# Performance work log

Measured on AMD Instinct MI355X. Metric: run time of the kernel, lower is better.

## Reference

```python
import jax, jax.numpy as jnp
import numpy as np

OUT_STEPS = 32
UNITS = 512
FEATURES = 64


def setup_inputs() -> dict:
    key = jax.random.key(0)
    ks = jax.random.split(key, 4)
    B, T, F, U = 2048, 128, FEATURES, UNITS
    scale = 0.05
    return {
        "inputs": jax.random.normal(ks[0], (B, T, F), dtype=jnp.float32),
        "W_x": jax.random.normal(ks[1], (F, 4 * U), dtype=jnp.float32) * scale,
        "W_h": jax.random.normal(ks[2], (U, 4 * U), dtype=jnp.float32) * scale,
        "b": jnp.zeros((4 * U,), dtype=jnp.float32),
        "dense_W": jax.random.normal(ks[3], (U, F), dtype=jnp.float32) * scale,
        "dense_b": jnp.zeros((F,), dtype=jnp.float32),
    }


def reference(inputs, W_x, W_h, b, dense_W, dense_b):
    U = W_h.shape[0]
    B = inputs.shape[0]

    def cell(h, c, x):
        # Keras LSTMCell: gates in i, f, g(c), o order
        z = x @ W_x + h @ W_h + b  # [B, 4U]
        i, f, g, o = jnp.split(z, 4, axis=-1)
        i = jax.nn.sigmoid(i)
        f = jax.nn.sigmoid(f)
        g = jnp.tanh(g)
        o = jax.nn.sigmoid(o)
        c2 = f * c + i * g
        h2 = o * jnp.tanh(c2)
        return h2, c2

    h0 = jnp.zeros((B, U), inputs.dtype)
    c0 = jnp.zeros((B, U), inputs.dtype)

    def warm_step(carry, x_t):
        h, c = carry
        h, c = cell(h, c, x_t)
        return (h, c), None

    (h, c), _ = jax.lax.scan(warm_step, (h0, c0), jnp.swapaxes(inputs, 0, 1))
    pred = h @ dense_W + dense_b  # [B, F]

    def dec_step(carry, _):
        p, hh, cc = carry
        hh, cc = cell(hh, cc, p)
        p2 = hh @ dense_W + dense_b
        return (p2, hh, cc), p2

    _, rest = jax.lax.scan(dec_step, (pred, h, c), None, length=OUT_STEPS - 1)
    preds = jnp.concatenate([pred[None], rest], axis=0)  # [out_steps, B, F]
    return jnp.swapaxes(preds, 0, 1)  # [B, out_steps, F]
```

## Files before the change

kernel.cpp:

```cpp
#include <hip/hip_runtime.h>
#include <hip/hip_bf16.h>

#define B_ 2048
#define T_ 128
#define F_ 64
#define U_ 512
#define FOURU 2048
#define OUTS 32
#define ROWS 128
#define COLSB 128
#define KTOT 576
#define LDSTR 584

typedef __attribute__((ext_vector_type(8))) short bf16x8;
typedef __attribute__((ext_vector_type(4))) float f32x4;

#define OFF_CNT   0
#define OFF_HBUF  20480
#define OFF_WT    (OFF_HBUF + 2*B_*U_*2)
#define OFF_WDEC  (OFF_WT + FOURU*KTOT*2)
#define OFF_DWT   (OFF_WDEC + FOURU*U_*2)
#define OFF_BDEC  (OFF_DWT + F_*U_*2)
#define OFF_XBF   (OFF_BDEC + FOURU*4)
#define WS_TOTAL  (OFF_XBF + (size_t)T_*B_*F_*2)

__device__ __forceinline__ short f2bf(float f) {
  union { float f; unsigned u; } a; a.f = f;
  unsigned u = a.u;
  unsigned r = u + 0x7FFFu + ((u >> 16) & 1u);
  return (short)(r >> 16);
}
__device__ __forceinline__ float sigm(float x){ return 1.0f/(1.0f+__expf(-x)); }
__device__ __forceinline__ float tanh_(float x){ return 1.0f - 2.0f/(1.0f+__expf(2.0f*x)); }

__global__ void prep_wt(const float* __restrict__ Wx, const float* __restrict__ Wh,
                        short* __restrict__ Wt) {
  int idx = blockIdx.x*256 + threadIdx.x;
  if (idx >= FOURU*KTOT) return;
  int c = idx / KTOT, k = idx % KTOT;
  float v = (k < F_) ? Wx[(size_t)k*FOURU + c] : Wh[(size_t)(k-F_)*FOURU + c];
  Wt[idx] = f2bf(v);
}
__global__ void prep_wdec(const float* __restrict__ Wh, const float* __restrict__ Wx,
                          const float* __restrict__ Dw, short* __restrict__ Wdec) {
  int idx = blockIdx.x*256 + threadIdx.x;
  if (idx >= FOURU*U_) return;
  int c = idx / U_, u = idx % U_;
  float a = Wh[(size_t)u*FOURU + c];
  for (int f=0; f<F_; ++f) a += Dw[u*F_ + f] * Wx[(size_t)f*FOURU + c];
  Wdec[idx] = f2bf(a);
}
__global__ void prep_bdec(const float* __restrict__ bv, const float* __restrict__ db,
                          const float* __restrict__ Wx, float* __restrict__ bdec) {
  int c = blockIdx.x*256 + threadIdx.x;
  if (c >= FOURU) return;
  float a = bv[c];
  for (int f=0; f<F_; ++f) a += db[f]*Wx[(size_t)f*FOURU + c];
  bdec[c] = a;
}
__global__ void prep_dwt(const float* __restrict__ Dw, short* __restrict__ Dwt) {
  int idx = blockIdx.x*256 + threadIdx.x;
  if (idx >= F_*U_) return;
  int f = idx / U_, u = idx % U_;
  Dwt[idx] = f2bf(Dw[u*F_ + f]);
}
__global__ void prep_x(const float* __restrict__ in, short* __restrict__ xbf) {
  int idx = blockIdx.x*256 + threadIdx.x;
  if (idx >= T_*B_*F_) return;
  int f = idx % F_, b = (idx / F_) % B_, t = idx / (F_*B_);
  xbf[idx] = f2bf(in[((size_t)b*T_ + t)*F_ + f]);
}

__global__ __launch_bounds__(1024, 4) void lstm_main(
    const short* __restrict__ xbf, const short* __restrict__ Wt,
    const short* __restrict__ Wdec, const short* __restrict__ Dwt,
    const float* __restrict__ bvec, const float* __restrict__ bdec,
    const float* __restrict__ dbv, short* hbuf, unsigned* cnt,
    float* __restrict__ out)
{
  __shared__ short wlds[COLSB*LDSTR];
  __shared__ int sSame;
  const int tid = threadIdx.x;
  const int bidx = blockIdx.x;
  const int gb = (bidx & 7)*2 + (bidx >> 7);
  const int gu = (bidx >> 3) & 15;

  unsigned* flags   = cnt + gb*256;
  unsigned* myFlag  = flags + gu*16;
  unsigned* regCnt  = cnt + 4096 + gb*16;
  unsigned* xcdTab  = cnt + 4352 + gb*16;
  unsigned* stepCnt = cnt + 4608 + gb*16;

  {
    unsigned xcc;
    asm volatile("s_getreg_b32 %0, hwreg(HW_REG_XCC_ID)" : "=s"(xcc));
    if (tid == 0) {
      __hip_atomic_store(&xcdTab[gu], xcc + 1u, __ATOMIC_RELAXED, __HIP_MEMORY_SCOPE_AGENT);
      __hip_atomic_fetch_add(regCnt, 1u, __ATOMIC_RELEASE, __HIP_MEMORY_SCOPE_AGENT);
      while (__hip_atomic_fetch_add(regCnt, 0u, __ATOMIC_RELAXED, __HIP_MEMORY_SCOPE_AGENT) < 16u)
        __builtin_amdgcn_s_sleep(1);
      __builtin_amdgcn_fence(__ATOMIC_ACQUIRE, "agent");
      unsigned x0 = __hip_atomic_load(&xcdTab[0], __ATOMIC_RELAXED, __HIP_MEMORY_SCOPE_AGENT);
      int same = 1;
      for (int i = 1; i < 16; ++i)
        same &= (__hip_atomic_load(&xcdTab[i], __ATOMIC_RELAXED, __HIP_MEMORY_SCOPE_AGENT) == x0);
      sSame = same;
    }
  }

  {
    const int c = tid >> 3, q = tid & 7;
    const int gate = (c >> 4) & 3;
    const int u = gu*32 + ((c >> 6) << 4) + (c & 15);
    const int gcol = gate*512 + u;
    const short* src = Wt + (size_t)gcol*KTOT + q*72;
    short* dst = wlds + c*LDSTR + q*72;
    #pragma unroll
    for (int j=0;j<9;j++)
      *(bf16x8*)(dst + j*8) = *(const bf16x8*)(src + j*8);
  }
  __syncthreads();
  const bool fastSync = (sSame != 0);

  const int w = tid >> 6, lane = tid & 63;
  const int wm = w >> 1, wn = w & 1;
  const int l15 = lane & 15, kh = lane >> 4;

  const int ucol = gu*32 + wn*16 + l15;
  float bia[4], biaD[4];
  #pragma unroll
  for (int g=0; g<4; ++g){ bia[g] = bvec[g*512 + ucol]; biaD[g] = bdec[g*512 + ucol]; }

  float cst[4] = {};
  const int rowA = gb*ROWS + wm*16 + l15;

  f32x4 acc[4];
  {
    const short* xp = xbf + ((size_t)0*B_ + rowA)*F_ + kh*8;
    bf16x8 a0 = *(const bf16x8*)(xp);
    bf16x8 a1 = *(const bf16x8*)(xp + 32);
    #pragma unroll
    for (int g=0; g<4; ++g) {
      bf16x8 b0 = *(const bf16x8*)(wlds + (size_t)(wn*64 + 16*g + l15)*LDSTR + kh*8);
      bf16x8 b1 = *(const bf16x8*)(wlds + (size_t)(wn*64 + 16*g + l15)*LDSTR + 32 + kh*8);
      f32x4 z = {0.f,0.f,0.f,0.f};
      z = __builtin_amdgcn_mfma_f32_16x16x32_bf16(a0, b0, z, 0,0,0);
      acc[g] = __builtin_amdgcn_mfma_f32_16x16x32_bf16(a1, b1, z, 0,0,0);
    }
  }

  for (int t = 0; t < 160; ++t) {
    if (t > 0) {
      if (fastSync) {
        if (tid < 64) {
          unsigned* fl = flags + (tid & 15)*16;
          for (;;) {
            unsigned v = __hip_atomic_load(fl, __ATOMIC_RELAXED, __HIP_MEMORY_SCOPE_AGENT);
            if (__ballot(v >= (unsigned)t) == ~0ull) break;
            __builtin_amdgcn_s_sleep(1);
          }
          asm volatile("buffer_inv sc0" ::: "memory");
          asm volatile("s_waitcnt vmcnt(0)" ::: "memory");
        }
      } else {
        if (tid == 0) {
          const unsigned target = 16u*(unsigned)t;
          while (__hip_atomic_fetch_add(stepCnt, 0u, __ATOMIC_RELAXED, __HIP_MEMORY_SCOPE_AGENT) < target)
            __builtin_amdgcn_s_sleep(1);
          __builtin_amdgcn_fence(__ATOMIC_ACQUIRE, "agent");
        }
      }
      __syncthreads();
    }

    if (t >= 128) {
      const int s = t - 128;
      if (gu < 8 && w < 4) {
        const short* hb = hbuf + (size_t)(t & 1)*B_*U_;
        const int pr0 = gb*ROWS + gu*16 + l15;
        f32x4 pa = {0.f,0.f,0.f,0.f};
        #pragma unroll
        for (int ks=0; ks<16; ++ks) {
          bf16x8 a = *(const bf16x8*)(hb + (size_t)pr0*U_ + ks*32 + kh*8);
          bf16x8 b = *(const bf16x8*)(Dwt + (size_t)(w*16 + l15)*U_ + ks*32 + kh*8);
          pa = __builtin_amdgcn_mfma_f32_16x16x32_bf16(a, b, pa, 0,0,0);
        }
        const int col = w*16 + l15;
        const float dbc = dbv[col];
        #pragma unroll
        for (int r=0; r<4; ++r) {
          const int orow = gb*ROWS + gu*16 + kh*4 + r;
          out[((size_t)orow*OUTS + s)*F_ + col] = pa[r] + dbc;
        }
      }
    }
    if (t == 159) break;
    if (t == 128) {
      __syncthreads();
      const int c = tid >> 3, q = tid & 7;
      const int gate = (c >> 4) & 3;
      const int u = gu*32 + ((c >> 6) << 4) + (c & 15);
      const int gcol = gate*512 + u;
      const short* src = Wdec + (size_t)gcol*U_ + q*64;
      short* dst = wlds + c*LDSTR + 64 + q*64;
      #pragma unroll
      for (int j=0;j<8;j++)
        *(bf16x8*)(dst + j*8) = *(const bf16x8*)(src + j*8);
      __syncthreads();
    }

    const short* hcur = hbuf + (size_t)(t & 1)*B_*U_;
    short* hnxt = hbuf + (size_t)((t+1) & 1)*B_*U_;
    {
      const short* hp = hcur + (size_t)rowA*U_ + kh*8;
      #pragma unroll
      for (int ks=0; ks<16; ++ks) {
        bf16x8 a = *(const bf16x8*)(hp + ks*32);
        #pragma unroll
        for (int g=0; g<4; ++g) {
          bf16x8 b = *(const bf16x8*)(wlds + (size_t)(wn*64 + 16*g + l15)*LDSTR + 64 + ks*32 + kh*8);
          acc[g] = __builtin_amdgcn_mfma_f32_16x16x32_bf16(a, b, acc[g], 0,0,0);
        }
      }
    }

    {
      const bool warm = (t < T_);
      #pragma unroll
      for (int r=0; r<4; ++r) {
        float zi = acc[0][r] + (warm ? bia[0] : biaD[0]);
        float zf = acc[1][r] + (warm ? bia[1] : biaD[1]);
        float zg = acc[2][r] + (warm ? bia[2] : biaD[2]);
        float zo = acc[3][r] + (warm ? bia[3] : biaD[3]);
        float ig = sigm(zi), fg = sigm(zf), gg = tanh_(zg), og = sigm(zo);
        float c2 = fmaf(fg, cst[r], ig*gg);
        cst[r] = c2;
        float h2 = og*tanh_(c2);
        const int row = gb*ROWS + wm*16 + kh*4 + r;
        hnxt[(size_t)row*U_ + ucol] = f2bf(h2);
      }
    }

    __syncthreads();
    if (tid == 0) {
      if (fastSync)
        __hip_atomic_store(myFlag, (unsigned)(t+1), __ATOMIC_RELAXED, __HIP_MEMORY_SCOPE_AGENT);
      else
        __hip_atomic_fetch_add(stepCnt, 1u, __ATOMIC_RELEASE, __HIP_MEMORY_SCOPE_AGENT);
    }

    if (t + 1 < T_) {
      const short* xp = xbf + ((size_t)(t+1)*B_ + rowA)*F_ + kh*8;
      bf16x8 a0 = *(const bf16x8*)(xp);
      bf16x8 a1 = *(const bf16x8*)(xp + 32);
      #pragma unroll
      for (int g=0; g<4; ++g) {
        bf16x8 b0 = *(const bf16x8*)(wlds + (size_t)(wn*64 + 16*g + l15)*LDSTR + kh*8);
        bf16x8 b1 = *(const bf16x8*)(wlds + (size_t)(wn*64 + 16*g + l15)*LDSTR + 32 + kh*8);
        f32x4 z = {0.f,0.f,0.f,0.f};
        z = __builtin_amdgcn_mfma_f32_16x16x32_bf16(a0, b0, z, 0,0,0);
        acc[g] = __builtin_amdgcn_mfma_f32_16x16x32_bf16(a1, b1, z, 0,0,0);
      }
    } else {
      #pragma unroll
      for (int g=0; g<4; ++g) acc[g] = (f32x4){0.f,0.f,0.f,0.f};
    }
  }
}

extern "C" void kernel_launch(void* const* d_in, const int* in_sizes, int n_in,
                              void* d_out, int out_size, void* d_ws, size_t ws_size,
                              hipStream_t stream) {
  const float* inputs = (const float*)d_in[0];
  const float* Wx = (const float*)d_in[1];
  const float* Wh = (const float*)d_in[2];
  const float* bv = (const float*)d_in[3];
  const float* Dw = (const float*)d_in[4];
  const float* db = (const float*)d_in[5];
  float* out = (float*)d_out;
  char* ws = (char*)d_ws;
  if (ws_size < WS_TOTAL) return;

  unsigned* cnt = (unsigned*)(ws + OFF_CNT);
  short* hbuf = (short*)(ws + OFF_HBUF);
  short* Wt   = (short*)(ws + OFF_WT);
  short* Wdec = (short*)(ws + OFF_WDEC);
  short* Dwt  = (short*)(ws + OFF_DWT);
  float* bdec = (float*)(ws + OFF_BDEC);
  short* xbf  = (short*)(ws + OFF_XBF);

  hipMemsetAsync(d_ws, 0, OFF_HBUF + (size_t)B_*U_*2, stream);
  prep_wt  <<<(FOURU*KTOT+255)/256, 256, 0, stream>>>(Wx, Wh, Wt);
  prep_wdec<<<(FOURU*U_ +255)/256, 256, 0, stream>>>(Wh, Wx, Dw, Wdec);
  prep_bdec<<<(FOURU     +255)/256, 256, 0, stream>>>(bv, db, Wx, bdec);
  prep_dwt <<<(F_*U_     +255)/256, 256, 0, stream>>>(Dw, Dwt);
  prep_x   <<<(T_*B_*F_  +255)/256, 256, 0, stream>>>(inputs, xbf);
  lstm_main<<<256, 1024, 0, stream>>>(xbf, Wt, Wdec, Dwt, bv, bdec, db, hbuf, cnt, out);
}
```

Measured before the change: 1.812 ms.

## Replace step barrier with per-slice flag waits and reshape LDS/wave tiling

```diff
diff --git a/kernel.cpp b/kernel.cpp
--- a/kernel.cpp
+++ b/kernel.cpp
@@ -7,10 +7,7 @@
 #define U_ 512
 #define FOURU 2048
 #define OUTS 32
-#define ROWS 128
-#define COLSB 128
 #define KTOT 576
-#define LDSTR 584
 
 typedef __attribute__((ext_vector_type(8))) short bf16x8;
 typedef __attribute__((ext_vector_type(4))) float f32x4;
@@ -33,6 +30,18 @@
 __device__ __forceinline__ float sigm(float x){ return 1.0f/(1.0f+__expf(-x)); }
 __device__ __forceinline__ float tanh_(float x){ return 1.0f - 2.0f/(1.0f+__expf(2.0f*x)); }
 
+template<int CTRL>
+__device__ __forceinline__ float dppb(float x) {
+  union { float f; int i; } a, b; a.f = x;
+  b.i = __builtin_amdgcn_mov_dpp(a.i, CTRL, 0xF, 0xF, true);
+  return b.f;
+}
+__device__ __forceinline__ float sel4(float x0, float x1, float x2, float x3, int qq) {
+  float lo = (qq & 1) ? x1 : x0;
+  float hi = (qq & 1) ? x3 : x2;
+  return (qq & 2) ? hi : lo;
+}
+
 __global__ void prep_wt(const float* __restrict__ Wx, const float* __restrict__ Wh,
                         short* __restrict__ Wt) {
   int idx = blockIdx.x*256 + threadIdx.x;
@@ -78,18 +87,17 @@
     const float* __restrict__ dbv, short* hbuf, unsigned* cnt,
     float* __restrict__ out)
 {
-  __shared__ short wlds[COLSB*LDSTR];
+  __shared__ short wlds[128*KTOT];
   __shared__ int sSame;
   const int tid = threadIdx.x;
   const int bidx = blockIdx.x;
   const int gb = (bidx & 7)*2 + (bidx >> 7);
   const int gu = (bidx >> 3) & 15;
 
-  unsigned* flags   = cnt + gb*256;
-  unsigned* myFlag  = flags + gu*16;
-  unsigned* regCnt  = cnt + 4096 + gb*16;
-  unsigned* xcdTab  = cnt + 4352 + gb*16;
-  unsigned* stepCnt = cnt + 4608 + gb*16;
+  unsigned* flags  = cnt + gb*256;
+  unsigned* myFlag = flags + gu*16;
+  unsigned* regCnt = cnt + 4096 + gb*16;
+  unsigned* xcdTab = cnt + 4352 + gb*16;
 
   {
     unsigned xcc;
@@ -109,135 +117,161 @@
   }
 
   {
-    const int c = tid >> 3, q = tid & 7;
-    const int gate = (c >> 4) & 3;
-    const int u = gu*32 + ((c >> 6) << 4) + (c & 15);
-    const int gcol = gate*512 + u;
-    const short* src = Wt + (size_t)gcol*KTOT + q*72;
-    short* dst = wlds + c*LDSTR + q*72;
-    #pragma unroll
-    for (int j=0;j<9;j++)
-      *(bf16x8*)(dst + j*8) = *(const bf16x8*)(src + j*8);
+    const int c = tid >> 3, q8 = tid & 7;
+    const int gcol = (c & 3)*512 + gu*32 + (c >> 2);
+    const int cx = c & 7;
+    #pragma unroll
+    for (int j = 0; j < 9; ++j) {
+      const int g = q8*9 + j;
+      *(bf16x8*)(wlds + (size_t)c*KTOT + (size_t)(g ^ cx)*8) =
+        *(const bf16x8*)(Wt + (size_t)gcol*KTOT + (size_t)g*8);
+    }
   }
   __syncthreads();
   const bool fastSync = (sSame != 0);
 
-  const int w = tid >> 6, lane = tid & 63;
-  const int wm = w >> 1, wn = w & 1;
+  const int w  = tid >> 6, lane = tid & 63;
+  const int wm = w >> 2, cq = w & 3;
   const int l15 = lane & 15, kh = lane >> 4;
-
-  const int ucol = gu*32 + wn*16 + l15;
-  float bia[4], biaD[4];
+  const int v = l15 >> 2, q = l15 & 3;
+  const int R0 = gb*128, U0 = gu*32;
+  const int cswz = l15 & 7;
+
+  float bia[2], biaD[2];
   #pragma unroll
-  for (int g=0; g<4; ++g){ bia[g] = bvec[g*512 + ucol]; biaD[g] = bdec[g*512 + ucol]; }
-
-  float cst[4] = {};
-  const int rowA = gb*ROWS + wm*16 + l15;
-
-  f32x4 acc[4];
-  {
-    const short* xp = xbf + ((size_t)0*B_ + rowA)*F_ + kh*8;
-    bf16x8 a0 = *(const bf16x8*)(xp);
-    bf16x8 a1 = *(const bf16x8*)(xp + 32);
-    #pragma unroll
-    for (int g=0; g<4; ++g) {
-      bf16x8 b0 = *(const bf16x8*)(wlds + (size_t)(wn*64 + 16*g + l15)*LDSTR + kh*8);
-      bf16x8 b1 = *(const bf16x8*)(wlds + (size_t)(wn*64 + 16*g + l15)*LDSTR + 32 + kh*8);
-      f32x4 z = {0.f,0.f,0.f,0.f};
-      z = __builtin_amdgcn_mfma_f32_16x16x32_bf16(a0, b0, z, 0,0,0);
-      acc[g] = __builtin_amdgcn_mfma_f32_16x16x32_bf16(a1, b1, z, 0,0,0);
-    }
+  for (int f = 0; f < 2; ++f) {
+    const int uc = U0 + cq*8 + f*4 + v;
+    bia[f]  = bvec[q*512 + uc];
+    biaD[f] = bdec[q*512 + uc];
   }
 
+  float cst[2][2] = {{0.f,0.f},{0.f,0.f}};
+  const int rowA = R0 + wm*32 + l15;
+
+  f32x4 acc[2][2];
+  #pragma unroll
+  for (int a = 0; a < 2; ++a)
+    #pragma unroll
+    for (int f = 0; f < 2; ++f) acc[a][f] = (f32x4){0.f,0.f,0.f,0.f};
+
+  auto do_x = [&](int tt) {
+    const short* xp = xbf + ((size_t)tt*B_ + rowA)*F_ + kh*8;
+    bf16x8 X0a = *(const bf16x8*)(xp);
+    bf16x8 X1a = *(const bf16x8*)(xp + 16*F_);
+    bf16x8 X0b = *(const bf16x8*)(xp + 32);
+    bf16x8 X1b = *(const bf16x8*)(xp + 16*F_ + 32);
+    #pragma unroll
+    for (int kx = 0; kx < 2; ++kx) {
+      const int gsw = (kx*4 + kh) ^ cswz;
+      bf16x8 B0 = *(const bf16x8*)(wlds + (size_t)(cq*32 + l15)*KTOT + (size_t)gsw*8);
+      bf16x8 B1 = *(const bf16x8*)(wlds + (size_t)(cq*32 + 16 + l15)*KTOT + (size_t)gsw*8);
+      bf16x8 Xa = kx ? X0b : X0a;
+      bf16x8 Xb = kx ? X1b : X1a;
+      acc[0][0] = __builtin_amdgcn_mfma_f32_16x16x32_bf16(Xa, B0, acc[0][0], 0,0,0);
+      acc[0][1] = __builtin_amdgcn_mfma_f32_16x16x32_bf16(Xa, B1, acc[0][1], 0,0,0);
+      acc[1][0] = __builtin_amdgcn_mfma_f32_16x16x32_bf16(Xb, B0, acc[1][0], 0,0,0);
+      acc[1][1] = __builtin_amdgcn_mfma_f32_16x16x32_bf16(Xb, B1, acc[1][1], 0,0,0);
+    }
+  };
+  do_x(0);
+
   for (int t = 0; t < 160; ++t) {
-    if (t > 0) {
-      if (fastSync) {
-        if (tid < 64) {
-          unsigned* fl = flags + (tid & 15)*16;
-          for (;;) {
-            unsigned v = __hip_atomic_load(fl, __ATOMIC_RELAXED, __HIP_MEMORY_SCOPE_AGENT);
-            if (__ballot(v >= (unsigned)t) == ~0ull) break;
-            __builtin_amdgcn_s_sleep(1);
+    if (t == 128) {
+      const int c = tid >> 3, q8 = tid & 7;
+      const int gcol = (c & 3)*512 + gu*32 + (c >> 2);
+      const int cx = c & 7;
+      #pragma unroll
+      for (int j = 0; j < 8; ++j) {
+        const int g = 8 + q8*8 + j;
+        *(bf16x8*)(wlds + (size_t)c*KTOT + (size_t)(g ^ cx)*8) =
+          *(const bf16x8*)(Wdec + (size_t)gcol*U_ + (size_t)(g-8)*8);
+      }
+      __syncthreads();
+    }
+
+    const short* hcur = hbuf + (size_t)(t & 1)*B_*U_;
+    short* hnxt = hbuf + (size_t)((t+1) & 1)*B_*U_;
+
+    asm volatile("buffer_inv sc0" ::: "memory");
+    asm volatile("s_waitcnt vmcnt(0)" ::: "memory");
+
+    unsigned fvq[2] = {0u, 0u};
+    if (fastSync) {
+      fvq[1] = __hip_atomic_load(&flags[((gu+1)&15)*16], __ATOMIC_RELAXED, __HIP_MEMORY_SCOPE_AGENT);
+      fvq[0] = __hip_atomic_load(&flags[((gu+2)&15)*16], __ATOMIC_RELAXED, __HIP_MEMORY_SCOPE_AGENT);
+    }
+    #pragma unroll
+    for (int i = 0; i < 16; ++i) {
+      const int ks = (gu + i) & 15;
+      if (i > 0) {
+        if (fastSync) {
+          unsigned vv = fvq[i & 1];
+          if (vv < (unsigned)t) {
+            const unsigned* fp = &flags[ks*16];
+            do {
+              __builtin_amdgcn_s_sleep(1);
+              vv = __hip_atomic_load(fp, __ATOMIC_RELAXED, __HIP_MEMORY_SCOPE_AGENT);
+            } while (vv < (unsigned)t);
           }
-          asm volatile("buffer_inv sc0" ::: "memory");
-          asm volatile("s_waitcnt vmcnt(0)" ::: "memory");
-        }
-      } else {
-        if (tid == 0) {
-          const unsigned target = 16u*(unsigned)t;
-          while (__hip_atomic_fetch_add(stepCnt, 0u, __ATOMIC_RELAXED, __HIP_MEMORY_SCOPE_AGENT) < target)
+        } else {
+          unsigned* fp = &flags[ks*16];
+          while (__hip_atomic_fetch_add(fp, 0u, __ATOMIC_RELAXED, __HIP_MEMORY_SCOPE_AGENT) < (unsigned)t)
             __builtin_amdgcn_s_sleep(1);
           __builtin_amdgcn_fence(__ATOMIC_ACQUIRE, "agent");
         }
-      }
-      __syncthreads();
-    }
-
-    if (t >= 128) {
-      const int s = t - 128;
-      if (gu < 8 && w < 4) {
-        const short* hb = hbuf + (size_t)(t & 1)*B_*U_;
-        const int pr0 = gb*ROWS + gu*16 + l15;
-        f32x4 pa = {0.f,0.f,0.f,0.f};
-        #pragma unroll
-        for (int ks=0; ks<16; ++ks) {
-          bf16x8 a = *(const bf16x8*)(hb + (size_t)pr0*U_ + ks*32 + kh*8);
-          bf16x8 b = *(const bf16x8*)(Dwt + (size_t)(w*16 + l15)*U_ + ks*32 + kh*8);
-          pa = __builtin_amdgcn_mfma_f32_16x16x32_bf16(a, b, pa, 0,0,0);
-        }
-        const int col = w*16 + l15;
-        const float dbc = dbv[col];
-        #pragma unroll
-        for (int r=0; r<4; ++r) {
-          const int orow = gb*ROWS + gu*16 + kh*4 + r;
-          out[((size_t)orow*OUTS + s)*F_ + col] = pa[r] + dbc;
-        }
-      }
-    }
-    if (t == 159) break;
-    if (t == 128) {
-      __syncthreads();
-      const int c = tid >> 3, q = tid & 7;
-      const int gate = (c >> 4) & 3;
-      const int u = gu*32 + ((c >> 6) << 4) + (c & 15);
-      const int gcol = gate*512 + u;
-      const short* src = Wdec + (size_t)gcol*U_ + q*64;
-      short* dst = wlds + c*LDSTR + 64 + q*64;
-      #pragma unroll
-      for (int j=0;j<8;j++)
-        *(bf16x8*)(dst + j*8) = *(const bf16x8*)(src + j*8);
-      __syncthreads();
-    }
-
-    const short* hcur = hbuf + (size_t)(t & 1)*B_*U_;
-    short* hnxt = hbuf + (size_t)((t+1) & 1)*B_*U_;
-    {
-      const short* hp = hcur + (size_t)rowA*U_ + kh*8;
-      #pragma unroll
-      for (int ks=0; ks<16; ++ks) {
-        bf16x8 a = *(const bf16x8*)(hp + ks*32);
-        #pragma unroll
-        for (int g=0; g<4; ++g) {
-          bf16x8 b = *(const bf16x8*)(wlds + (size_t)(wn*64 + 16*g + l15)*LDSTR + 64 + ks*32 + kh*8);
-          acc[g] = __builtin_amdgcn_mfma_f32_16x16x32_bf16(a, b, acc[g], 0,0,0);
-        }
-      }
+        asm volatile("" ::: "memory");
+      }
+      const short* hp = hcur + (size_t)rowA*U_ + ks*32 + kh*8;
+      bf16x8 A0 = *(const bf16x8*)(hp);
+      bf16x8 A1 = *(const bf16x8*)(hp + 16*U_);
+      if (fastSync && i >= 1 && i < 14)
+        fvq[i & 1] = __hip_atomic_load(&flags[((gu+i+2)&15)*16], __ATOMIC_RELAXED, __HIP_MEMORY_SCOPE_AGENT);
+      const int gsw = (8 + ks*4 + kh) ^ cswz;
+      bf16x8 B0 = *(const bf16x8*)(wlds + (size_t)(cq*32 + l15)*KTOT + (size_t)gsw*8);
+      bf16x8 B1 = *(const bf16x8*)(wlds + (size_t)(cq*32 + 16 + l15)*KTOT + (size_t)gsw*8);
+      acc[0][0] = __builtin_amdgcn_mfma_f32_16x16x32_bf16(A0, B0, acc[0][0], 0,0,0);
+      acc[0][1] = __builtin_amdgcn_mfma_f32_16x16x32_bf16(A0, B1, acc[0][1], 0,0,0);
+      acc[1][0] = __builtin_amdgcn_mfma_f32_16x16x32_bf16(A1, B0, acc[1][0], 0,0,0);
+      acc[1][1] = __builtin_amdgcn_mfma_f32_16x16x32_bf16(A1, B1, acc[1][1], 0,0,0);
     }
 
     {
       const bool warm = (t < T_);
       #pragma unroll
-      for (int r=0; r<4; ++r) {
-        float zi = acc[0][r] + (warm ? bia[0] : biaD[0]);
-        float zf = acc[1][r] + (warm ? bia[1] : biaD[1]);
-        float zg = acc[2][r] + (warm ? bia[2] : biaD[2]);
-        float zo = acc[3][r] + (warm ? bia[3] : biaD[3]);
+      for (int a = 0; a < 2; ++a)
+      #pragma unroll
+      for (int f = 0; f < 2; ++f) {
+        const float bb = warm ? bia[f] : biaD[f];
+        float z0 = acc[a][f][0] + bb, z1 = acc[a][f][1] + bb;
+        float z2 = acc[a][f][2] + bb, z3 = acc[a][f][3] + bb;
+        float zi = sel4(dppb<0x00>(z0), dppb<0x00>(z1), dppb<0x00>(z2), dppb<0x00>(z3), q);
+        float zf = sel4(dppb<0x55>(z0), dppb<0x55>(z1), dppb<0x55>(z2), dppb<0x55>(z3), q);
+        float zg = sel4(dppb<0xAA>(z0), dppb<0xAA>(z1), dppb<0xAA>(z2), dppb<0xAA>(z3), q);
+        float zo = sel4(dppb<0xFF>(z0), dppb<0xFF>(z1), dppb<0xFF>(z2), dppb<0xFF>(z3), q);
         float ig = sigm(zi), fg = sigm(zf), gg = tanh_(zg), og = sigm(zo);
-        float c2 = fmaf(fg, cst[r], ig*gg);
-        cst[r] = c2;
+        float c2 = fmaf(fg, cst[a][f], ig*gg);
+        cst[a][f] = c2;
         float h2 = og*tanh_(c2);
-        const int row = gb*ROWS + wm*16 + kh*4 + r;
-        hnxt[(size_t)row*U_ + ucol] = f2bf(h2);
+        hnxt[(size_t)(R0 + wm*32 + a*16 + kh*4 + q)*U_ + U0 + cq*8 + f*4 + v] = f2bf(h2);
+      }
+    }
+
+    if (t >= 128 && gu < 8 && w < 4) {
+      const int s = t - 128;
+      const int pr0 = R0 + gu*16 + l15;
+      f32x4 pa = {0.f,0.f,0.f,0.f};
+      #pragma unroll
+      for (int ks2 = 0; ks2 < 16; ++ks2) {
+        bf16x8 a2 = *(const bf16x8*)(hcur + (size_t)pr0*U_ + ks2*32 + kh*8);
+        bf16x8 b2 = *(const bf16x8*)(Dwt + (size_t)(w*16 + l15)*U_ + ks2*32 + kh*8);
+        pa = __builtin_amdgcn_mfma_f32_16x16x32_bf16(a2, b2, pa, 0,0,0);
+      }
+      const int col = w*16 + l15;
+      const float dbc = dbv[col];
+      #pragma unroll
+      for (int r = 0; r < 4; ++r) {
+        const int orow = R0 + gu*16 + kh*4 + r;
+        out[((size_t)orow*OUTS + s)*F_ + col] = pa[r] + dbc;
       }
     }
 
@@ -246,25 +280,14 @@
       if (fastSync)
         __hip_atomic_store(myFlag, (unsigned)(t+1), __ATOMIC_RELAXED, __HIP_MEMORY_SCOPE_AGENT);
       else
-        __hip_atomic_fetch_add(stepCnt, 1u, __ATOMIC_RELEASE, __HIP_MEMORY_SCOPE_AGENT);
-    }
-
-    if (t + 1 < T_) {
-      const short* xp = xbf + ((size_t)(t+1)*B_ + rowA)*F_ + kh*8;
-      bf16x8 a0 = *(const bf16x8*)(xp);
-      bf16x8 a1 = *(const bf16x8*)(xp + 32);
-      #pragma unroll
-      for (int g=0; g<4; ++g) {
-        bf16x8 b0 = *(const bf16x8*)(wlds + (size_t)(wn*64 + 16*g + l15)*LDSTR + kh*8);
-        bf16x8 b1 = *(const bf16x8*)(wlds + (size_t)(wn*64 + 16*g + l15)*LDSTR + 32 + kh*8);
-        f32x4 z = {0.f,0.f,0.f,0.f};
-        z = __builtin_amdgcn_mfma_f32_16x16x32_bf16(a0, b0, z, 0,0,0);
-        acc[g] = __builtin_amdgcn_mfma_f32_16x16x32_bf16(a1, b1, z, 0,0,0);
-      }
-    } else {
-      #pragma unroll
-      for (int g=0; g<4; ++g) acc[g] = (f32x4){0.f,0.f,0.f,0.f};
-    }
+        __hip_atomic_fetch_add(myFlag, 1u, __ATOMIC_RELEASE, __HIP_MEMORY_SCOPE_AGENT);
+    }
+
+    #pragma unroll
+    for (int a = 0; a < 2; ++a)
+      #pragma unroll
+      for (int f = 0; f < 2; ++f) acc[a][f] = (f32x4){0.f,0.f,0.f,0.f};
+    if (t + 1 < T_) do_x(t+1);
   }
 }
 
```

After: 3.126 ms. +72.6%, slower.

## Triple-buffer hidden state and move dense projection after step signal

Applied to the files above, without the earlier changes.

```diff
diff --git a/kernel.cpp b/kernel.cpp
--- a/kernel.cpp
+++ b/kernel.cpp
@@ -17,7 +17,7 @@
 
 #define OFF_CNT   0
 #define OFF_HBUF  20480
-#define OFF_WT    (OFF_HBUF + 2*B_*U_*2)
+#define OFF_WT    (OFF_HBUF + 3*B_*U_*2)
 #define OFF_WDEC  (OFF_WT + FOURU*KTOT*2)
 #define OFF_DWT   (OFF_WDEC + FOURU*U_*2)
 #define OFF_BDEC  (OFF_DWT + F_*U_*2)
@@ -85,11 +85,10 @@
   const int gb = (bidx & 7)*2 + (bidx >> 7);
   const int gu = (bidx >> 3) & 15;
 
-  unsigned* flags   = cnt + gb*256;
-  unsigned* myFlag  = flags + gu*16;
-  unsigned* regCnt  = cnt + 4096 + gb*16;
-  unsigned* xcdTab  = cnt + 4352 + gb*16;
-  unsigned* stepCnt = cnt + 4608 + gb*16;
+  unsigned* flags  = cnt + gb*256;
+  unsigned* myFlag = flags + gu*16;
+  unsigned* regCnt = cnt + 4096 + gb*16;
+  unsigned* xcdTab = cnt + 4352 + gb*16;
 
   {
     unsigned xcc;
@@ -134,9 +133,19 @@
   float cst[4] = {};
   const int rowA = gb*ROWS + wm*16 + l15;
 
+  bf16x8 Bc[4][4];
+  auto loadBc = [&]() {
+    #pragma unroll
+    for (int ks=0; ks<4; ++ks)
+      #pragma unroll
+      for (int g=0; g<4; ++g)
+        Bc[ks][g] = *(const bf16x8*)(wlds + (size_t)(wn*64 + 16*g + l15)*LDSTR + 64 + ks*32 + kh*8);
+  };
+  loadBc();
+
   f32x4 acc[4];
-  {
-    const short* xp = xbf + ((size_t)0*B_ + rowA)*F_ + kh*8;
+  auto do_x = [&](int tt) {
+    const short* xp = xbf + ((size_t)tt*B_ + rowA)*F_ + kh*8;
     bf16x8 a0 = *(const bf16x8*)(xp);
     bf16x8 a1 = *(const bf16x8*)(xp + 32);
     #pragma unroll
@@ -147,7 +156,8 @@
       z = __builtin_amdgcn_mfma_f32_16x16x32_bf16(a0, b0, z, 0,0,0);
       acc[g] = __builtin_amdgcn_mfma_f32_16x16x32_bf16(a1, b1, z, 0,0,0);
     }
-  }
+  };
+  do_x(0);
 
   for (int t = 0; t < 160; ++t) {
     if (t > 0) {
@@ -155,116 +165,110 @@
         if (tid < 64) {
           unsigned* fl = flags + (tid & 15)*16;
           for (;;) {
-            unsigned v = __hip_atomic_load(fl, __ATOMIC_RELAXED, __HIP_MEMORY_SCOPE_AGENT);
-            if (__ballot(v >= (unsigned)t) == ~0ull) break;
+            unsigned vv = __hip_atomic_load(fl, __ATOMIC_RELAXED, __HIP_MEMORY_SCOPE_AGENT);
+            if (__ballot(vv >= (unsigned)t) == ~0ull) break;
             __builtin_amdgcn_s_sleep(1);
           }
           asm volatile("buffer_inv sc0" ::: "memory");
           asm volatile("s_waitcnt vmcnt(0)" ::: "memory");
         }
       } else {
-        if (tid == 0) {
-          const unsigned target = 16u*(unsigned)t;
-          while (__hip_atomic_fetch_add(stepCnt, 0u, __ATOMIC_RELAXED, __HIP_MEMORY_SCOPE_AGENT) < target)
+        if (tid < 64) {
+          unsigned* fl = flags + (tid & 15)*16;
+          for (;;) {
+            unsigned vv = __hip_atomic_fetch_add(fl, 0u, __ATOMIC_RELAXED, __HIP_MEMORY_SCOPE_AGENT);
+            if (__ballot(vv >= (unsigned)t) == ~0ull) break;
             __builtin_amdgcn_s_sleep(1);
+          }
+        }
+        if (tid == 0)
           __builtin_amdgcn_fence(__ATOMIC_ACQUIRE, "agent");
-        }
       }
       __syncthreads();
     }
 
-    if (t >= 128) {
-      const int s = t - 128;
-      if (gu < 8 && w < 4) {
-        const short* hb = hbuf + (size_t)(t & 1)*B_*U_;
-        const int pr0 = gb*ROWS + gu*16 + l15;
-        f32x4 pa = {0.f,0.f,0.f,0.f};
+    const int cur = t % 3;
+    const short* hcur = hbuf + (size_t)cur*B_*U_;
+
+    if (t < 159) {
+      if (t == 128) {
+        const int c = tid >> 3, q = tid & 7;
+        const int gate = (c >> 4) & 3;
+        const int u = gu*32 + ((c >> 6) << 4) + (c & 15);
+        const int gcol = gate*512 + u;
+        const short* src = Wdec + (size_t)gcol*U_ + q*64;
+        short* dst = wlds + c*LDSTR + 64 + q*64;
+        #pragma unroll
+        for (int j=0;j<8;j++)
+          *(bf16x8*)(dst + j*8) = *(const bf16x8*)(src + j*8);
+        __syncthreads();
+        loadBc();
+      }
+
+      short* hnxt = hbuf + (size_t)((t+1) % 3)*B_*U_;
+
+      {
+        const short* hp = hcur + (size_t)rowA*U_ + kh*8;
         #pragma unroll
         for (int ks=0; ks<16; ++ks) {
-          bf16x8 a = *(const bf16x8*)(hb + (size_t)pr0*U_ + ks*32 + kh*8);
-          bf16x8 b = *(const bf16x8*)(Dwt + (size_t)(w*16 + l15)*U_ + ks*32 + kh*8);
-          pa = __builtin_amdgcn_mfma_f32_16x16x32_bf16(a, b, pa, 0,0,0);
+          bf16x8 a = *(const bf16x8*)(hp + ks*32);
+          #pragma unroll
+          for (int g=0; g<4; ++g) {
+            bf16x8 b = (ks < 4) ? Bc[ks][g]
+              : *(const bf16x8*)(wlds + (size_t)(wn*64 + 16*g + l15)*LDSTR + 64 + ks*32 + kh*8);
+            acc[g] = __builtin_amdgcn_mfma_f32_16x16x32_bf16(a, b, acc[g], 0,0,0);
+          }
         }
-        const int col = w*16 + l15;
-        const float dbc = dbv[col];
+      }
+
+      {
+        const bool warm = (t < T_);
         #pragma unroll
         for (int r=0; r<4; ++r) {
-          const int orow = gb*ROWS + gu*16 + kh*4 + r;
-          out[((size_t)orow*OUTS + s)*F_ + col] = pa[r] + dbc;
+          float zi = acc[0][r] + (warm ? bia[0] : biaD[0]);
+          float zf = acc[1][r] + (warm ? bia[1] : biaD[1]);
+          float zg = acc[2][r] + (warm ? bia[2] : biaD[2]);
+          float zo = acc[3][r] + (warm ? bia[3] : biaD[3]);
+          float ig = sigm(zi), fg = sigm(zf), gg = tanh_(zg), og = sigm(zo);
+          float c2 = fmaf(fg, cst[r], ig*gg);
+          cst[r] = c2;
+          float h2 = og*tanh_(c2);
+          const int row = gb*ROWS + wm*16 + kh*4 + r;
+          hnxt[(size_t)row*U_ + ucol] = f2bf(h2);
         }
       }
-    }
-    if (t == 159) break;
-    if (t == 128) {
+
       __syncthreads();
-      const int c = tid >> 3, q = tid & 7;
-      const int gate = (c >> 4) & 3;
-      const int u = gu*32 + ((c >> 6) << 4) + (c & 15);
-      const int gcol = gate*512 + u;
-      const short* src = Wdec + (size_t)gcol*U_ + q*64;
-      short* dst = wlds + c*LDSTR + 64 + q*64;
-      #pragma unroll
-      for (int j=0;j<8;j++)
-        *(bf16x8*)(dst + j*8) = *(const bf16x8*)(src + j*8);
-      __syncthreads();
-    }
-
-    const short* hcur = hbuf + (size_t)(t & 1)*B_*U_;
-    short* hnxt = hbuf + (size_t)((t+1) & 1)*B_*U_;
-    {
-      const short* hp = hcur + (size_t)rowA*U_ + kh*8;
+      if (tid == 0) {
+        if (fastSync)
+          __hip_atomic_store(myFlag, (unsigned)(t+1), __ATOMIC_RELAXED, __HIP_MEMORY_SCOPE_AGENT);
+        else
+          __hip_atomic_fetch_add(myFlag, 1u, __ATOMIC_RELEASE, __HIP_MEMORY_SCOPE_AGENT);
+      }
+    }
+
+    if (t >= 128 && gu < 8 && w < 4) {
+      const int s = t - 128;
+      const int pr0 = gb*ROWS + gu*16 + l15;
+      f32x4 pa = {0.f,0.f,0.f,0.f};
       #pragma unroll
       for (int ks=0; ks<16; ++ks) {
-        bf16x8 a = *(const bf16x8*)(hp + ks*32);
-        #pragma unroll
-        for (int g=0; g<4; ++g) {
-          bf16x8 b = *(const bf16x8*)(wlds + (size_t)(wn*64 + 16*g + l15)*LDSTR + 64 + ks*32 + kh*8);
-          acc[g] = __builtin_amdgcn_mfma_f32_16x16x32_bf16(a, b, acc[g], 0,0,0);
-        }
-      }
-    }
-
-    {
-      const bool warm = (t < T_);
+        bf16x8 a = *(const bf16x8*)(hcur + (size_t)pr0*U_ + ks*32 + kh*8);
+        bf16x8 b = *(const bf16x8*)(Dwt + (size_t)(w*16 + l15)*U_ + ks*32 + kh*8);
+        pa = __builtin_amdgcn_mfma_f32_16x16x32_bf16(a, b, pa, 0,0,0);
+      }
+      const int col = w*16 + l15;
+      const float dbc = dbv[col];
       #pragma unroll
       for (int r=0; r<4; ++r) {
-        float zi = acc[0][r] + (warm ? bia[0] : biaD[0]);
-        float zf = acc[1][r] + (warm ? bia[1] : biaD[1]);
-        float zg = acc[2][r] + (warm ? bia[2] : biaD[2]);
-        float zo = acc[3][r] + (warm ? bia[3] : biaD[3]);
-        float ig = sigm(zi), fg = sigm(zf), gg = tanh_(zg), og = sigm(zo);
-        float c2 = fmaf(fg, cst[r], ig*gg);
-        cst[r] = c2;
-        float h2 = og*tanh_(c2);
-        const int row = gb*ROWS + wm*16 + kh*4 + r;
-        hnxt[(size_t)row*U_ + ucol] = f2bf(h2);
-      }
-    }
-
-    __syncthreads();
-    if (tid == 0) {
-      if (fastSync)
-        __hip_atomic_store(myFlag, (unsigned)(t+1), __ATOMIC_RELAXED, __HIP_MEMORY_SCOPE_AGENT);
-      else
-        __hip_atomic_fetch_add(stepCnt, 1u, __ATOMIC_RELEASE, __HIP_MEMORY_SCOPE_AGENT);
-    }
-
-    if (t + 1 < T_) {
-      const short* xp = xbf + ((size_t)(t+1)*B_ + rowA)*F_ + kh*8;
-      bf16x8 a0 = *(const bf16x8*)(xp);
-      bf16x8 a1 = *(const bf16x8*)(xp + 32);
-      #pragma unroll
-      for (int g=0; g<4; ++g) {
-        bf16x8 b0 = *(const bf16x8*)(wlds + (size_t)(wn*64 + 16*g + l15)*LDSTR + kh*8);
-        bf16x8 b1 = *(const bf16x8*)(wlds + (size_t)(wn*64 + 16*g + l15)*LDSTR + 32 + kh*8);
-        f32x4 z = {0.f,0.f,0.f,0.f};
-        z = __builtin_amdgcn_mfma_f32_16x16x32_bf16(a0, b0, z, 0,0,0);
-        acc[g] = __builtin_amdgcn_mfma_f32_16x16x32_bf16(a1, b1, z, 0,0,0);
-      }
-    } else {
-      #pragma unroll
-      for (int g=0; g<4; ++g) acc[g] = (f32x4){0.f,0.f,0.f,0.f};
-    }
+        const int orow = gb*ROWS + gu*16 + kh*4 + r;
+        out[((size_t)orow*OUTS + s)*F_ + col] = pa[r] + dbc;
+      }
+    }
+
+    #pragma unroll
+    for (int g=0; g<4; ++g) acc[g] = (f32x4){0.f,0.f,0.f,0.f};
+    if (t + 1 < T_) do_x(t+1);
   }
 }
 
```

New measurement: 1.996 ms. 10.2% more time.
